# Kernel optimization log

Measured on AMD Instinct MI355X. Metric: run time of the kernel, lower is better.

The kernel has to match this reference:

```python
import jax, jax.numpy as jnp
import numpy as np

B, N, D = 8, 4096, 256
Q, C = 8, 1024


def setup_inputs() -> dict:
    key = jax.random.key(0)
    k1, k2 = jax.random.split(key)
    x = jax.random.normal(k1, (B, N, D), dtype=jnp.float32)
    codebooks = jax.random.normal(k2, (Q, C, D), dtype=jnp.float32)
    return {"x": x, "codebooks": codebooks}


def reference(x, codebooks):
    """Residual VQ (Algorithm 1, https://arxiv.org/pdf/2107.03312.pdf).
    x: [B, N, D] tokens. codebooks: [Q, C, D], one euclidean codebook per stage.
    Returns (quantized_out [B,N,D], indices [B,N,Q], losses [Q]).
    Eval-mode math: nearest-neighbor lookup, straight-through estimator,
    commitment loss = mse(stop_grad(quantized), residual)."""

    def step(carry, cb):
        residual, qout = carry  # each [B, N, D]
        # squared L2 distances to codebook: [B, N, C]
        d2 = (
            jnp.sum(residual * residual, axis=-1, keepdims=True)
            - 2.0 * jnp.einsum("bnd,cd->bnc", residual, cb)
            + jnp.sum(cb * cb, axis=-1)
        )
        idx = jnp.argmin(d2, axis=-1)  # [B, N] int32
        q = cb[idx]  # gather: [B, N, D]
        loss = jnp.mean((jax.lax.stop_gradient(q) - residual) ** 2)
        # straight-through: forward value q, gradient flows to residual
        q_st = residual + jax.lax.stop_gradient(q - residual)
        return (residual - q_st, qout + q_st), (idx, loss)

    (_, qout), (indices, losses) = jax.lax.scan(
        step, (x, jnp.zeros_like(x)), codebooks
    )
    # stack along last dim, like torch.stack(dim=-1)
    indices = jnp.moveaxis(indices, 0, -1)  # [B, N, Q]
    return qout, indices, losses
```

## Files before the change

kernel.cpp:

```cpp
#include <hip/hip_runtime.h>

typedef __attribute__((ext_vector_type(8))) short short8;
typedef __attribute__((ext_vector_type(4))) float f32x4;

constexpr int Bq = 8, Nn = 4096, Dd = 256, Qq = 8, Cc = 1024;
constexpr int Mm = Bq * Nn;
constexpr int TOK = 64;
constexpr int NT = 512;
constexpr int LCAP = 32;
constexpr float MARGIN = 0.5f;

__device__ inline unsigned short f2bf(float f) {
  unsigned u = __float_as_uint(f);
  unsigned r = (u + 0x7FFFu + ((u >> 16) & 1u)) >> 16;
  return (unsigned short)r;
}
__device__ inline float bf2f(unsigned short h) { return __uint_as_float(((unsigned)h) << 16); }
__device__ inline unsigned fenc(float f) {
  unsigned u = __float_as_uint(f);
  return (u & 0x80000000u) ? ~u : (u | 0x80000000u);
}
__device__ inline float fdec(unsigned e) {
  unsigned u = (e & 0x80000000u) ? (e & 0x7fffffffu) : ~e;
  return __uint_as_float(u);
}

__global__ void prep_kernel(const float* __restrict__ cbs,
                            float* __restrict__ cnorm,
                            float* __restrict__ loss_acc) {
  const int wave = threadIdx.x >> 6;
  const int lane = threadIdx.x & 63;
  const int row  = blockIdx.x * 4 + wave;
  const float4* r4 = reinterpret_cast<const float4*>(cbs + (size_t)row * Dd);
  const float4 v = r4[lane];
  float s = v.x * v.x + v.y * v.y + v.z * v.z + v.w * v.w;
#pragma unroll
  for (int off = 32; off; off >>= 1) s += __shfl_down(s, off);
  if (lane == 0) cnorm[row] = s;
  if (blockIdx.x == 0 && threadIdx.x < Qq) loss_acc[threadIdx.x] = 0.0f;
}

__global__ __launch_bounds__(256)
void build_bfrag(const float* __restrict__ cbs, short* __restrict__ Bh) {
  const int q    = blockIdx.x >> 6;
  const int nt   = blockIdx.x & 63;
  const int lane = threadIdx.x & 63;
  const int ks0  = threadIdx.x >> 6;
#pragma unroll
  for (int h = 0; h < 2; ++h) {
    const int ks = ks0 + h * 4;
    const int c  = nt * 16 + (lane & 15);
    const int k  = ks * 32 + (lane >> 4) * 8;
    const float* src = cbs + ((size_t)(q * Cc + c)) * Dd + k;
    short8 hi;
#pragma unroll
    for (int j = 0; j < 8; ++j) hi[j] = (short)f2bf(src[j]);
    ((short8*)Bh)[(((size_t)(q * 64 + nt) * 8 + ks) * 64 + lane)] = hi;
  }
}

__device__ float exact_score_lds(const float4* __restrict__ tile, int t, int sw,
                                 const float* __restrict__ cb,
                                 const float* __restrict__ cnorm, int cand) {
  const float4* cv = reinterpret_cast<const float4*>(cb + (size_t)cand * Dd);
  float a = 0.0f;
#pragma unroll 8
  for (int d4 = 0; d4 < 64; ++d4) {
    const float4 rv = tile[(t * 64 + d4) ^ sw];
    const float4 c4 = cv[d4];
    a += rv.x * c4.x; a += rv.y * c4.y; a += rv.z * c4.z; a += rv.w * c4.w;
  }
  return cnorm[cand] - 2.0f * a;
}

__global__ __launch_bounds__(NT, 1)
void vq_fused(const float* __restrict__ cbs,
              const short8* __restrict__ bh,
              const float* __restrict__ cnorm,
              const float* __restrict__ x,
              float* __restrict__ qout,
              float* __restrict__ idx_out,
              float* __restrict__ loss_acc) {
  __shared__ short8 bbuf[8][8][64];
  __shared__ float4 tile[TOK * 64];
  __shared__ float  cn_lds[Cc];
  __shared__ unsigned runm_sh[TOK];
  __shared__ int cnt[TOK];
  __shared__ int list[TOK][LCAP];
  __shared__ int win[TOK];

  const int tid  = threadIdx.x;
  const int lane = tid & 63;
  const int wv   = tid >> 6;
  const int tg   = wv >> 1;
  const int h    = wv & 1;
  const int tok0 = blockIdx.x * TOK;
  const int col  = lane & 15;
  const int g4   = lane >> 4;

  const float4* xs = reinterpret_cast<const float4*>(x + (size_t)tok0 * Dd);
#pragma unroll
  for (int k = 0; k < 8; ++k) {
    const int j = tid + k * NT;
    const int tk = j >> 6, d4 = j & 63;
    tile[(tk * 64 + d4) ^ (tk & 7)] = xs[j];
  }
  __syncthreads();

  auto stage_oct = [&](const short8* bhq, int oct) {
#pragma unroll
    for (int i = 0; i < 8; ++i) {
      const int c  = wv * 8 + i;
      const int t  = c >> 3, ks = c & 7;
      const short8* src = bhq + (((size_t)(oct * 8 + t)) * 8 + ks) * 64 + lane;
      short8* dst = &bbuf[t][ks][0];
      __builtin_amdgcn_global_load_lds(
          (const __attribute__((address_space(1))) void*)src,
          (__attribute__((address_space(3))) void*)dst, 16, 0, 0);
    }
  };

  stage_oct(bh, 0);

#pragma unroll 1
  for (int q = 0; q < Qq; ++q) {
    const float*  cb  = cbs + (size_t)q * Cc * Dd;
    const float*  cn_ = cnorm + (size_t)q * Cc;
    const short8* bhq = bh + (size_t)q * 32768;

    short8 ah[8], al[8];
    {
      const int tk = tg * 16 + (lane & 15);
      const int sw = tk & 7;
#pragma unroll
      for (int ks = 0; ks < 8; ++ks) {
        const int d4 = ks * 8 + (lane >> 4) * 2;
        const float4 f0 = tile[(tk * 64 + d4) ^ sw];
        const float4 f1 = tile[(tk * 64 + d4 + 1) ^ sw];
        const float v[8] = {f0.x, f0.y, f0.z, f0.w, f1.x, f1.y, f1.z, f1.w};
#pragma unroll
        for (int j = 0; j < 8; ++j) {
          const unsigned short hb = f2bf(v[j]);
          ah[ks][j] = (short)hb;
          al[ks][j] = (short)f2bf(v[j] - bf2f(hb));
        }
      }
    }
    if (tid < TOK) { cnt[tid] = 0; runm_sh[tid] = fenc(3.4e38f); }
    if (tid < 256) {
      const float4* s4 = reinterpret_cast<const float4*>(cn_);
      reinterpret_cast<float4*>(cn_lds)[tid] = s4[tid];
    }

    float min8[4];
#pragma unroll
    for (int r = 0; r < 4; ++r) min8[r] = 3.4e38f;

#pragma unroll 1
    for (int o = 0; o < 8; ++o) {
      __syncthreads();

      float s[4][4];
#pragma unroll
      for (int pair = 0; pair < 2; ++pair) {
        f32x4 acc[2][2];
#pragma unroll
        for (int tp = 0; tp < 2; ++tp)
#pragma unroll
          for (int pp = 0; pp < 2; ++pp) acc[tp][pp] = (f32x4){0.f, 0.f, 0.f, 0.f};
#pragma unroll
        for (int ks = 0; ks < 8; ++ks) {
#pragma unroll
          for (int tp = 0; tp < 2; ++tp) {
            const short8 vb = bbuf[h * 4 + pair * 2 + tp][ks][lane];
            acc[tp][0] = __builtin_amdgcn_mfma_f32_16x16x32_bf16(ah[ks], vb, acc[tp][0], 0, 0, 0);
            acc[tp][1] = __builtin_amdgcn_mfma_f32_16x16x32_bf16(al[ks], vb, acc[tp][1], 0, 0, 0);
          }
        }
#pragma unroll
        for (int tp = 0; tp < 2; ++tp) {
          const float cn = cn_lds[(o * 8 + h * 4 + pair * 2 + tp) * 16 + col];
#pragma unroll
          for (int r = 0; r < 4; ++r) {
            s[pair * 2 + tp][r] = cn - 2.0f * (acc[tp][0][r] + acc[tp][1][r]);
            min8[r] = s[pair * 2 + tp][r] < min8[r] ? s[pair * 2 + tp][r] : min8[r];
          }
        }
      }
      __syncthreads();

      if (o + 1 < 8)       stage_oct(bhq, o + 1);
      else if (q + 1 < Qq) stage_oct(bhq + 32768, 0);

      if (o == 0 || o == 3 || o == 7) {
#pragma unroll
        for (int r = 0; r < 4; ++r) {
          float v = min8[r];
#pragma unroll
          for (int m = 1; m < 16; m <<= 1) {
            const float ov = __shfl_xor(v, m);
            v = ov < v ? ov : v;
          }
          if (col == 0)
            atomicMin(&runm_sh[tg * 16 + g4 * 4 + r], fenc(v));
        }
      }

#pragma unroll
      for (int jt = 0; jt < 4; ++jt)
#pragma unroll
        for (int r = 0; r < 4; ++r) {
          const int t = tg * 16 + g4 * 4 + r;
          if (s[jt][r] <= fdec(runm_sh[t]) + MARGIN) {
            const int pos = atomicAdd(&cnt[t], 1);
            if (pos < LCAP) list[t][pos] = (o * 8 + h * 4 + jt) * 16 + col;
          }
        }
    }
    __syncthreads();

    {
      const int t    = tid >> 3;
      const int slot = tid & 7;
      const int sw   = t & 7;
      const int c_   = cnt[t];
      float best = 3.4e38f;
      int   wdx  = 1 << 30;
      if (c_ == 1) {
        wdx = list[t][0];
        best = 0.0f;
      } else if (c_ <= LCAP) {
        for (int it = slot; it < c_; it += 8) {
          const int cand = list[t][it];
          const float sc = exact_score_lds(tile, t, sw, cb, cn_, cand);
          if (sc < best || (sc == best && cand < wdx)) { best = sc; wdx = cand; }
        }
      } else {
        for (int cand = slot; cand < Cc; cand += 8) {
          const float sc = exact_score_lds(tile, t, sw, cb, cn_, cand);
          if (sc < best || (sc == best && cand < wdx)) { best = sc; wdx = cand; }
        }
      }
#pragma unroll
      for (int m = 1; m < 8; m <<= 1) {
        const float ov = __shfl_xor(best, m);
        const int   oi = __shfl_xor(wdx, m);
        if (ov < best || (ov == best && oi < wdx)) { best = ov; wdx = oi; }
      }
      if (slot == 0) {
        win[t] = wdx;
        idx_out[(size_t)(tok0 + t) * Qq + q] = (float)wdx;
      }
    }
    __syncthreads();

    float lsum = 0.0f;
    {
      const float4* cb4 = reinterpret_cast<const float4*>(cb);
#pragma unroll
      for (int k = 0; k < 8; ++k) {
        const int j = tid + k * NT;
        const int tk = j >> 6, d4 = j & 63;
        const int widx = win[tk];
        const float4 cv = cb4[(size_t)widx * 64 + d4];
        const float4 rv = tile[(tk * 64 + d4) ^ (tk & 7)];
        const float ex = cv.x - rv.x, ey = cv.y - rv.y, ez = cv.z - rv.z, ew = cv.w - rv.w;
        const float qsx = rv.x + ex, qsy = rv.y + ey, qsz = rv.z + ez, qsw = rv.w + ew;
        lsum += ex * ex + ey * ey + ez * ez + ew * ew;
        tile[(tk * 64 + d4) ^ (tk & 7)] =
            make_float4(rv.x - qsx, rv.y - qsy, rv.z - qsz, rv.w - qsw);
      }
    }
#pragma unroll
    for (int s = 32; s; s >>= 1) lsum += __shfl_xor(lsum, s);
    if (lane == 0) atomicAdd(&loss_acc[q], lsum);
    __syncthreads();
  }

  {
    float4* qo = reinterpret_cast<float4*>(qout + (size_t)tok0 * Dd);
#pragma unroll
    for (int k = 0; k < 8; ++k) {
      const int j = tid + k * NT;
      const int tk = j >> 6, d4 = j & 63;
      const float4 xv = xs[j];
      const float4 rv = tile[(tk * 64 + d4) ^ (tk & 7)];
      qo[j] = make_float4(xv.x - rv.x, xv.y - rv.y, xv.z - rv.z, xv.w - rv.w);
    }
  }
}

__global__ void finalize_losses(const float* __restrict__ loss_acc,
                                float* __restrict__ loss_out) {
  if (threadIdx.x < Qq) loss_out[threadIdx.x] = loss_acc[threadIdx.x] * (1.0f / (float)(Mm * Dd));
}

extern "C" void kernel_launch(void* const* d_in, const int* in_sizes, int n_in,
                              void* d_out, int out_size, void* d_ws, size_t ws_size,
                              hipStream_t stream) {
  const float* x   = (const float*)d_in[0];
  const float* cbs = (const float*)d_in[1];
  float* out      = (float*)d_out;
  float* qout     = out;
  float* idx_out  = out + (size_t)Mm * Dd;
  float* loss_out = idx_out + (size_t)Mm * Qq;

  char* w = (char*)d_ws;
  short* Bh       = (short*)w;
  float* cnorm    = (float*)(w + (size_t)4194304);
  float* loss_acc = (float*)(w + (size_t)4227072);

  prep_kernel<<<(Qq * Cc) / 4, 256, 0, stream>>>(cbs, cnorm, loss_acc);
  build_bfrag<<<Qq * 64, 256, 0, stream>>>(cbs, Bh);

  vq_fused<<<Mm / TOK, NT, 0, stream>>>(cbs, (const short8*)Bh,
                                        cnorm, x, qout, idx_out, loss_acc);

  finalize_losses<<<1, 64, 0, stream>>>(loss_acc, loss_out);
}
```

Measured before the change: 658.1 us.

## Move residual tile from LDS to global workspace to allow two blocks per CU

Removes the 64 KB per-block LDS residual tile and keeps the residual in a global scratch buffer instead. Each stage reads it from global memory (x on stage 0) and writes the updated residual back, with the final stage writing qout directly. Launch bounds are raised to two blocks per CU so the smaller LDS footprint can admit more resident blocks. The cost is extra global/L2 traffic for residual reads in the A-fragment build, the exact rescoring and the update, plus a tighter register budget.

New measurement: 833.2 us. +26.6%, slower.

```diff
diff --git a/kernel.cpp b/kernel.cpp
--- a/kernel.cpp
+++ b/kernel.cpp
@@ -59,30 +59,30 @@
   }
 }
 
-__device__ float exact_score_lds(const float4* __restrict__ tile, int t, int sw,
-                                 const float* __restrict__ cb,
-                                 const float* __restrict__ cnorm, int cand) {
+__device__ float exact_score_g(const float4* __restrict__ rv4,
+                               const float* __restrict__ cb,
+                               const float* __restrict__ cnorm, int cand) {
   const float4* cv = reinterpret_cast<const float4*>(cb + (size_t)cand * Dd);
   float a = 0.0f;
 #pragma unroll 8
   for (int d4 = 0; d4 < 64; ++d4) {
-    const float4 rv = tile[(t * 64 + d4) ^ sw];
+    const float4 rv = rv4[d4];
     const float4 c4 = cv[d4];
     a += rv.x * c4.x; a += rv.y * c4.y; a += rv.z * c4.z; a += rv.w * c4.w;
   }
   return cnorm[cand] - 2.0f * a;
 }
 
-__global__ __launch_bounds__(NT, 1)
+__global__ __launch_bounds__(NT, 2)
 void vq_fused(const float* __restrict__ cbs,
               const short8* __restrict__ bh,
               const float* __restrict__ cnorm,
               const float* __restrict__ x,
+              float* __restrict__ rbuf,
               float* __restrict__ qout,
               float* __restrict__ idx_out,
               float* __restrict__ loss_acc) {
   __shared__ short8 bbuf[8][8][64];
-  __shared__ float4 tile[TOK * 64];
   __shared__ float  cn_lds[Cc];
   __shared__ unsigned runm_sh[TOK];
   __shared__ int cnt[TOK];
@@ -98,15 +98,6 @@
   const int col  = lane & 15;
   const int g4   = lane >> 4;
 
-  const float4* xs = reinterpret_cast<const float4*>(x + (size_t)tok0 * Dd);
-#pragma unroll
-  for (int k = 0; k < 8; ++k) {
-    const int j = tid + k * NT;
-    const int tk = j >> 6, d4 = j & 63;
-    tile[(tk * 64 + d4) ^ (tk & 7)] = xs[j];
-  }
-  __syncthreads();
-
   auto stage_oct = [&](const short8* bhq, int oct) {
 #pragma unroll
     for (int i = 0; i < 8; ++i) {
@@ -127,16 +118,16 @@
     const float*  cb  = cbs + (size_t)q * Cc * Dd;
     const float*  cn_ = cnorm + (size_t)q * Cc;
     const short8* bhq = bh + (size_t)q * 32768;
+    const float*  rq  = (q == 0) ? x : rbuf;
 
     short8 ah[8], al[8];
     {
       const int tk = tg * 16 + (lane & 15);
-      const int sw = tk & 7;
+      const float* rbase = rq + (size_t)(tok0 + tk) * Dd + (lane >> 4) * 8;
 #pragma unroll
       for (int ks = 0; ks < 8; ++ks) {
-        const int d4 = ks * 8 + (lane >> 4) * 2;
-        const float4 f0 = tile[(tk * 64 + d4) ^ sw];
-        const float4 f1 = tile[(tk * 64 + d4 + 1) ^ sw];
+        const float4 f0 = *reinterpret_cast<const float4*>(rbase + ks * 32);
+        const float4 f1 = *reinterpret_cast<const float4*>(rbase + ks * 32 + 4);
         const float v[8] = {f0.x, f0.y, f0.z, f0.w, f1.x, f1.y, f1.z, f1.w};
 #pragma unroll
         for (int j = 0; j < 8; ++j) {
@@ -222,7 +213,7 @@
     {
       const int t    = tid >> 3;
       const int slot = tid & 7;
-      const int sw   = t & 7;
+      const float4* rv4 = reinterpret_cast<const float4*>(rq + (size_t)(tok0 + t) * Dd);
       const int c_   = cnt[t];
       float best = 3.4e38f;
       int   wdx  = 1 << 30;
@@ -232,12 +223,12 @@
       } else if (c_ <= LCAP) {
         for (int it = slot; it < c_; it += 8) {
           const int cand = list[t][it];
-          const float sc = exact_score_lds(tile, t, sw, cb, cn_, cand);
+          const float sc = exact_score_g(rv4, cb, cn_, cand);
           if (sc < best || (sc == best && cand < wdx)) { best = sc; wdx = cand; }
         }
       } else {
         for (int cand = slot; cand < Cc; cand += 8) {
-          const float sc = exact_score_lds(tile, t, sw, cb, cn_, cand);
+          const float sc = exact_score_g(rv4, cb, cn_, cand);
           if (sc < best || (sc == best && cand < wdx)) { best = sc; wdx = cand; }
         }
       }
@@ -256,37 +247,34 @@
 
     float lsum = 0.0f;
     {
-      const float4* cb4 = reinterpret_cast<const float4*>(cb);
+      const float4* cb4  = reinterpret_cast<const float4*>(cb);
+      const float4* rp   = reinterpret_cast<const float4*>(rq + (size_t)tok0 * Dd);
+      const float4* xs   = reinterpret_cast<const float4*>(x + (size_t)tok0 * Dd);
+      float4* rw = reinterpret_cast<float4*>(rbuf + (size_t)tok0 * Dd);
+      float4* qo = reinterpret_cast<float4*>(qout + (size_t)tok0 * Dd);
 #pragma unroll
       for (int k = 0; k < 8; ++k) {
         const int j = tid + k * NT;
         const int tk = j >> 6, d4 = j & 63;
         const int widx = win[tk];
         const float4 cv = cb4[(size_t)widx * 64 + d4];
-        const float4 rv = tile[(tk * 64 + d4) ^ (tk & 7)];
+        const float4 rv = rp[j];
         const float ex = cv.x - rv.x, ey = cv.y - rv.y, ez = cv.z - rv.z, ew = cv.w - rv.w;
         const float qsx = rv.x + ex, qsy = rv.y + ey, qsz = rv.z + ez, qsw = rv.w + ew;
         lsum += ex * ex + ey * ey + ez * ez + ew * ew;
-        tile[(tk * 64 + d4) ^ (tk & 7)] =
-            make_float4(rv.x - qsx, rv.y - qsy, rv.z - qsz, rv.w - qsw);
+        const float4 rn = make_float4(rv.x - qsx, rv.y - qsy, rv.z - qsz, rv.w - qsw);
+        if (q == Qq - 1) {
+          const float4 xv = xs[j];
+          qo[j] = make_float4(xv.x - rn.x, xv.y - rn.y, xv.z - rn.z, xv.w - rn.w);
+        } else {
+          rw[j] = rn;
+        }
       }
     }
 #pragma unroll
     for (int s = 32; s; s >>= 1) lsum += __shfl_xor(lsum, s);
     if (lane == 0) atomicAdd(&loss_acc[q], lsum);
     __syncthreads();
-  }
-
-  {
-    float4* qo = reinterpret_cast<float4*>(qout + (size_t)tok0 * Dd);
-#pragma unroll
-    for (int k = 0; k < 8; ++k) {
-      const int j = tid + k * NT;
-      const int tk = j >> 6, d4 = j & 63;
-      const float4 xv = xs[j];
-      const float4 rv = tile[(tk * 64 + d4) ^ (tk & 7)];
-      qo[j] = make_float4(xv.x - rv.x, xv.y - rv.y, xv.z - rv.z, xv.w - rv.w);
-    }
   }
 }
 
@@ -306,15 +294,16 @@
   float* loss_out = idx_out + (size_t)Mm * Qq;
 
   char* w = (char*)d_ws;
-  short* Bh       = (short*)w;
-  float* cnorm    = (float*)(w + (size_t)4194304);
-  float* loss_acc = (float*)(w + (size_t)4227072);
+  float* rbuf     = (float*)w;
+  short* Bh       = (short*)(w + (size_t)33554432);
+  float* cnorm    = (float*)(w + (size_t)37748736);
+  float* loss_acc = (float*)(w + (size_t)37781504);
 
   prep_kernel<<<(Qq * Cc) / 4, 256, 0, stream>>>(cbs, cnorm, loss_acc);
   build_bfrag<<<Qq * 64, 256, 0, stream>>>(cbs, Bh);
 
   vq_fused<<<Mm / TOK, NT, 0, stream>>>(cbs, (const short8*)Bh,
-                                        cnorm, x, qout, idx_out, loss_acc);
+                                        cnorm, x, rbuf, qout, idx_out, loss_acc);
 
   finalize_losses<<<1, 64, 0, stream>>>(loss_acc, loss_out);
 }
```
